# Performance work log

Measured on AMD Instinct MI355X. Metric: run time of the kernel, lower is better.

The kernel has to match this reference:

```python
import jax, jax.numpy as jnp
import numpy as np

GRAPH_SIZES = [864, 1728, 3456, 6912]
VERTEX_NUM = 6890
B, NZ, FC_DIM = 128, 128, 512
CH = [128, 128, 64, 32, 16]
EDGE_FACTOR = 6  # directed edges per node (triangle mesh)
LRELU = 0.2


def setup_inputs() -> dict:
    key = jax.random.key(0)
    ks = jax.random.split(key, 24)
    s = 0.02
    inp = {
        'x': jax.random.normal(ks[0], (B, NZ), jnp.float32),
        'fc_w1': s * jax.random.normal(ks[1], (NZ, FC_DIM), jnp.float32),
        'fc_b1': jnp.zeros((FC_DIM,), jnp.float32),
        'fc_w2': s * jax.random.normal(ks[2], (FC_DIM, GRAPH_SIZES[0] * CH[0]), jnp.float32),
        'fc_b2': jnp.zeros((GRAPH_SIZES[0] * CH[0],), jnp.float32),
    }
    # Chebyshev weights [K=3, C_in, C_out] per layer (+ final conv to 3)
    cio = [(CH[0], CH[1]), (CH[1], CH[2]), (CH[2], CH[3]), (CH[3], CH[4]), (CH[4], 3)]
    for i, (ci, co) in enumerate(cio):
        inp[f'W{i}'] = s * jax.random.normal(ks[3 + i], (3, ci, co), jnp.float32)
        inp[f'b{i}'] = jnp.zeros((co,), jnp.float32)
    # fixed edge lists per level
    for i, n in enumerate(GRAPH_SIZES):
        e = EDGE_FACTOR * n
        inp[f'edge{i}'] = jax.random.randint(ks[10 + i], (2, e), 0, n, dtype=jnp.int64)
    inp['perm_back'] = jax.random.randint(ks[20], (GRAPH_SIZES[-1],), 0, GRAPH_SIZES[-1], dtype=jnp.int64)
    return inp


def cheb_conv(x, edge_index, W, b, num_nodes):
    # PyG-style ChebConv with lambda_max=2: L_hat = L - I = -D^{-1/2} A D^{-1/2}
    src, dst = edge_index[0], edge_index[1]
    deg = jnp.zeros((num_nodes,), x.dtype).at[dst].add(jnp.ones(src.shape, x.dtype))
    dinv = jnp.where(deg > 0, 1.0 / jnp.sqrt(jnp.maximum(deg, 1.0)), 0.0)
    norm = -(dinv[src] * dinv[dst])  # [E]

    def prop(h):  # h: [B, N, C] -> L_hat @ h (gather + scatter-add over edges)
        msg = h[:, src, :] * norm[None, :, None]
        return jnp.zeros_like(h).at[:, dst, :].add(msg)

    Tx0 = x
    Tx1 = prop(Tx0)
    Tx2 = 2.0 * prop(Tx1) - Tx0
    out = (jnp.einsum('bnc,co->bno', Tx0, W[0])
           + jnp.einsum('bnc,co->bno', Tx1, W[1])
           + jnp.einsum('bnc,co->bno', Tx2, W[2]))
    return out + b


def lrelu(x):
    return jnp.where(x >= 0, x, LRELU * x)


def reference(x, fc_w1, fc_b1, fc_w2, fc_b2,
              W0, b0, W1, b1, W2, b2, W3, b3, W4, b4,
              edge0, edge1, edge2, edge3, perm_back):
    h = jax.nn.relu(x @ fc_w1 + fc_b1)
    h = h @ fc_w2 + fc_b2                      # dropout = identity (eval mode)
    h = h.reshape(h.shape[0], GRAPH_SIZES[0], -1)  # [B, 864, 128]
    edges = [edge0, edge1, edge2, edge3]
    Ws = [(W0, b0), (W1, b1), (W2, b2), (W3, b3)]
    for i in range(4):
        h = lrelu(cheb_conv(h, edges[i], Ws[i][0], Ws[i][1], GRAPH_SIZES[i]))
        if i < 3:
            h = jnp.repeat(h, 2, axis=1)       # Upsample(scale_factor=2) along nodes
    h = cheb_conv(h, edge3, W4, b4, GRAPH_SIZES[3])  # final conv to 3 coords
    h = h[:, perm_back, :]                      # perm_data gather
    return h[:, :VERTEX_NUM, :]
```

## Files before the change

kernel.cpp:

```cpp
#include <hip/hip_runtime.h>
#include <hip/hip_bf16.h>

#define DEVFN __device__ __forceinline__

__global__ void k_signal(float* out, float v) {
    if (threadIdx.x == 0 && blockIdx.x == 0) out[0] = v;
}

__global__ void k_detect64(const long long* __restrict__ p, int count, int* flag) {
    if (threadIdx.x == 0 && blockIdx.x == 0) {
        int ok = 1;
        for (int i = 0; i < count; i++) {
            long long v = p[i];
            if (v < 0 || v >= (1LL << 30)) { ok = 0; break; }
        }
        *flag = ok;
    }
}

__global__ __launch_bounds__(256) void k_cvt_idx(const void* __restrict__ p, int n,
                                                 const int* __restrict__ flag,
                                                 int* __restrict__ out) {
    int i = blockIdx.x * 256 + threadIdx.x;
    if (i >= n) return;
    if (*flag) out[i] = (int)((const long long*)p)[i];
    else       out[i] = ((const int*)p)[i];
}

__global__ __launch_bounds__(256) void k_fc1(const float* __restrict__ x,
                                             const float* __restrict__ w,
                                             const float* __restrict__ b,
                                             float* __restrict__ out) {
    int j = blockIdx.x * 256 + threadIdx.x;
    int m = blockIdx.y;
    float acc = b[j];
    const float* xr = x + m * 128;
    for (int k = 0; k < 128; k++)
        acc = fmaf(xr[k], w[k * 512 + j], acc);
    out[j * 128 + m] = fmaxf(acc, 0.f);
}

__global__ __launch_bounds__(256) void k_fc2_gemm4(const float* __restrict__ h1t,
                                                   const float* __restrict__ w,
                                                   const float* __restrict__ bias,
                                                   float* __restrict__ out) {
    const int N = 110592, K = 512;
    constexpr int KT = 32, NT = 128;
    __shared__ float At[KT * 128];
    __shared__ float Bt[KT * NT];

    const int tid = threadIdx.x;
    const int cg = tid & 15;
    const int rg = tid >> 4;
    const int nbase = blockIdx.x * NT;
    const int r0 = rg * 8;
    const int c0 = cg * 4;

    float acc[8][8];
#pragma unroll
    for (int j = 0; j < 4; j++) {
        float bj0 = bias[nbase + c0 + j];
        float bj1 = bias[nbase + 64 + c0 + j];
#pragma unroll
        for (int r = 0; r < 8; r++) { acc[r][j] = bj0; acc[r][j + 4] = bj1; }
    }

    for (int k0 = 0; k0 < K; k0 += KT) {
        __syncthreads();
#pragma unroll
        for (int it = 0; it < 4; it++) {
            int idx = tid + it * 256;
            int kk = idx >> 5, r4 = (idx & 31) * 4;
            *(float4*)(At + kk * 128 + r4) =
                *(const float4*)(h1t + (size_t)(k0 + kk) * 128 + r4);
        }
#pragma unroll
        for (int it = 0; it < 4; it++) {
            int idx = tid + it * 256;
            int kk = idx >> 5, c4 = (idx & 31) * 4;
            *(float4*)(Bt + kk * NT + c4) =
                *(const float4*)(w + (size_t)(k0 + kk) * N + nbase + c4);
        }
        __syncthreads();
#pragma unroll 8
        for (int k = 0; k < KT; k++) {
            float4 a0 = *(const float4*)(At + k * 128 + r0);
            float4 a1 = *(const float4*)(At + k * 128 + r0 + 4);
            float4 b0 = *(const float4*)(Bt + k * NT + c0);
            float4 b1 = *(const float4*)(Bt + k * NT + c0 + 64);
            float av[8] = {a0.x, a0.y, a0.z, a0.w, a1.x, a1.y, a1.z, a1.w};
            float bv[8] = {b0.x, b0.y, b0.z, b0.w, b1.x, b1.y, b1.z, b1.w};
#pragma unroll
            for (int r = 0; r < 8; r++)
#pragma unroll
                for (int j = 0; j < 8; j++)
                    acc[r][j] = fmaf(av[r], bv[j], acc[r][j]);
        }
    }

#pragma unroll
    for (int r = 0; r < 8; r++) {
        int m = r0 + r;
        float4 o0 = {acc[r][0], acc[r][1], acc[r][2], acc[r][3]};
        float4 o1 = {acc[r][4], acc[r][5], acc[r][6], acc[r][7]};
        *(float4*)(out + (size_t)m * N + nbase + c0) = o0;
        *(float4*)(out + (size_t)m * N + nbase + c0 + 64) = o1;
    }
}

__global__ __launch_bounds__(256) void k_zero_int(int* p, int n) {
    int i = blockIdx.x * 256 + threadIdx.x;
    if (i < n) p[i] = 0;
}

__global__ __launch_bounds__(256) void k_deg(const int* __restrict__ dst, int e,
                                             int* __restrict__ deg) {
    int i = blockIdx.x * 256 + threadIdx.x;
    if (i < e) atomicAdd(&deg[dst[i]], 1);
}

__global__ __launch_bounds__(256) void k_dinv(const int* __restrict__ deg,
                                              float* __restrict__ dinv, int n) {
    int i = blockIdx.x * 256 + threadIdx.x;
    if (i < n) dinv[i] = deg[i] > 0 ? 1.0f / sqrtf((float)deg[i]) : 0.0f;
}

__global__ __launch_bounds__(256) void k_scan(const int* __restrict__ deg,
                                              int* __restrict__ row_ptr, int n) {
    __shared__ int part[256];
    int tid = threadIdx.x;
    int per = (n + 255) / 256;
    int start = tid * per;
    int end = min(start + per, n);
    int s = 0;
    for (int i = start; i < end; i++) s += deg[i];
    part[tid] = s;
    __syncthreads();
    for (int off = 1; off < 256; off <<= 1) {
        int t = (tid >= off) ? part[tid - off] : 0;
        __syncthreads();
        part[tid] += t;
        __syncthreads();
    }
    int base = (tid == 0) ? 0 : part[tid - 1];
    int run = base;
    for (int i = start; i < end; i++) { row_ptr[i] = run; run += deg[i]; }
    if (tid == 255) row_ptr[n] = part[255];
}

__global__ __launch_bounds__(256) void k_fill(const int* __restrict__ src,
                                              const int* __restrict__ dst, int e,
                                              const int* __restrict__ row_ptr,
                                              int* __restrict__ cnt,
                                              const float* __restrict__ dinv,
                                              int* __restrict__ col, float* __restrict__ val) {
    int i = blockIdx.x * 256 + threadIdx.x;
    if (i >= e) return;
    int d = dst[i], s = src[i];
    int slot = row_ptr[d] + atomicAdd(&cnt[d], 1);
    col[slot] = s;
    val[slot] = -dinv[s] * dinv[d];
}

template <int CI, int MODE>
__global__ __launch_bounds__(256) void k_prop2(const float* __restrict__ h,
                                               const float* __restrict__ sub,
                                               const int* __restrict__ row_ptr,
                                               const int* __restrict__ col,
                                               const float* __restrict__ val,
                                               float* __restrict__ out, int n) {
    constexpr int C4 = CI / 4;
    constexpr int BY = 256 / C4;
    int c4 = threadIdx.x;
    int d = blockIdx.x;
    int b = blockIdx.y * BY + threadIdx.y;
    int p0 = row_ptr[d], p1 = row_ptr[d + 1];
    float4 acc = {0.f, 0.f, 0.f, 0.f};
    const float4* hb = (const float4*)h + (size_t)b * n * C4;
    for (int p = p0; p < p1; p++) {
        float vp = val[p];
        float4 hv = hb[(size_t)col[p] * C4 + c4];
        acc.x = fmaf(vp, hv.x, acc.x);
        acc.y = fmaf(vp, hv.y, acc.y);
        acc.z = fmaf(vp, hv.z, acc.z);
        acc.w = fmaf(vp, hv.w, acc.w);
    }
    size_t oi = ((size_t)b * n + d) * C4 + c4;
    if (MODE) {
        float4 s = ((const float4*)sub)[oi];
        acc.x = 2.f * acc.x - s.x;
        acc.y = 2.f * acc.y - s.y;
        acc.z = 2.f * acc.z - s.z;
        acc.w = 2.f * acc.w - s.w;
    }
    ((float4*)out)[oi] = acc;
}

template <int CI, int CO, bool REPEAT>
__global__ __launch_bounds__(256) void k_cheb_gemm3(const float* __restrict__ t0,
                                                    const float* __restrict__ t1,
                                                    const float* __restrict__ t2,
                                                    const float* __restrict__ W,
                                                    const float* __restrict__ bias,
                                                    float* __restrict__ out, int n) {
    constexpr int CGN = CO / 8;
    constexpr int MT = 1024 / CGN;
    constexpr int KT = 32, AST = 37;
    __shared__ float At[MT * AST];
    __shared__ float Wt_s[KT * CO];

    const int tid = threadIdx.x;
    const int cg = tid % CGN;
    const int rg = tid / CGN;
    const int m_base = blockIdx.x * MT;
    const int c0 = cg * 8;

    float acc[4][8];
#pragma unroll
    for (int jj = 0; jj < 8; jj++) {
        float bj = bias[c0 + jj];
#pragma unroll
        for (int r = 0; r < 4; r++) acc[r][jj] = bj;
    }

    const float* As[3] = {t0, t1, t2};
#pragma unroll 1
    for (int t = 0; t < 3; t++) {
        const float* A = As[t];
        const float* Wg = W + t * CI * CO;
#pragma unroll 1
        for (int k0 = 0; k0 < CI; k0 += KT) {
            __syncthreads();
#pragma unroll
            for (int it = 0; it < MT / 32; it++) {
                int idx = tid + it * 256;
                int row = idx >> 3, k4 = (idx & 7) * 4;
                float4 a = *(const float4*)(A + (size_t)(m_base + row) * CI + k0 + k4);
                float* dst = At + row * AST + k4;
                dst[0] = a.x; dst[1] = a.y; dst[2] = a.z; dst[3] = a.w;
            }
#pragma unroll
            for (int it = 0; it < (KT * CO) / 1024; it++) {
                int idx = tid + it * 256;
                int kk = idx / (CO / 4), c4 = (idx % (CO / 4)) * 4;
                *(float4*)(Wt_s + kk * CO + c4) =
                    *(const float4*)(Wg + (k0 + kk) * CO + c4);
            }
            __syncthreads();
#pragma unroll 4
            for (int k = 0; k < KT; k++) {
                float a0 = At[(rg * 4 + 0) * AST + k];
                float a1 = At[(rg * 4 + 1) * AST + k];
                float a2 = At[(rg * 4 + 2) * AST + k];
                float a3 = At[(rg * 4 + 3) * AST + k];
                float4 w0 = *(const float4*)(Wt_s + k * CO + c0);
                float4 w1 = *(const float4*)(Wt_s + k * CO + c0 + 4);
                float wv[8] = {w0.x, w0.y, w0.z, w0.w, w1.x, w1.y, w1.z, w1.w};
#pragma unroll
                for (int jj = 0; jj < 8; jj++) {
                    acc[0][jj] = fmaf(a0, wv[jj], acc[0][jj]);
                    acc[1][jj] = fmaf(a1, wv[jj], acc[1][jj]);
                    acc[2][jj] = fmaf(a2, wv[jj], acc[2][jj]);
                    acc[3][jj] = fmaf(a3, wv[jj], acc[3][jj]);
                }
            }
        }
    }

#pragma unroll
    for (int r = 0; r < 4; r++) {
        int m = m_base + rg * 4 + r;
#pragma unroll
        for (int jj = 0; jj < 8; jj++) {
            float v = acc[r][jj];
            acc[r][jj] = v >= 0.f ? v : 0.2f * v;
        }
        float4 o0 = {acc[r][0], acc[r][1], acc[r][2], acc[r][3]};
        float4 o1 = {acc[r][4], acc[r][5], acc[r][6], acc[r][7]};
        if (REPEAT) {
            int b = m / n, d = m - (m / n) * n;
            size_t ob = ((size_t)b * (2 * n) + 2 * d) * CO + c0;
            *(float4*)(out + ob) = o0;
            *(float4*)(out + ob + 4) = o1;
            *(float4*)(out + ob + CO) = o0;
            *(float4*)(out + ob + CO + 4) = o1;
        } else {
            *(float4*)(out + (size_t)m * CO + c0) = o0;
            *(float4*)(out + (size_t)m * CO + c0 + 4) = o1;
        }
    }
}

__global__ __launch_bounds__(256) void k_cheb_small(const float* __restrict__ t0,
                                                    const float* __restrict__ t1,
                                                    const float* __restrict__ t2,
                                                    const float* __restrict__ W,
                                                    const float* __restrict__ bias,
                                                    float* __restrict__ out) {
    constexpr int CI = 32, CO = 16, MT = 256, AST = 33;
    __shared__ float At[MT * AST];
    __shared__ float Ws[3 * CI * CO];

    const int tid = threadIdx.x;
    const int cg = tid & 1;
    const int rg = tid >> 1;
    const int c0 = cg * 8;
    const int m_base = blockIdx.x * MT;

    for (int i = tid; i < 384; i += 256)
        ((float4*)Ws)[i] = ((const float4*)W)[i];

    float acc[2][8];
#pragma unroll
    for (int jj = 0; jj < 8; jj++) {
        float bj = bias[c0 + jj];
        acc[0][jj] = bj; acc[1][jj] = bj;
    }

    const float* As[3] = {t0, t1, t2};
#pragma unroll 1
    for (int t = 0; t < 3; t++) {
        const float* A = As[t];
        __syncthreads();
#pragma unroll
        for (int it = 0; it < 8; it++) {
            int idx = tid + it * 256;
            int row = idx >> 3, k4 = (idx & 7) * 4;
            float4 a = *(const float4*)(A + (size_t)(m_base + row) * CI + k4);
            float* dst = At + row * AST + k4;
            dst[0] = a.x; dst[1] = a.y; dst[2] = a.z; dst[3] = a.w;
        }
        __syncthreads();
        const float* Wt = Ws + t * CI * CO;
#pragma unroll 8
        for (int k = 0; k < CI; k++) {
            float a0 = At[rg * AST + k];
            float a1 = At[(rg + 128) * AST + k];
            float4 w0 = *(const float4*)(Wt + k * CO + c0);
            float4 w1 = *(const float4*)(Wt + k * CO + c0 + 4);
            float wv[8] = {w0.x, w0.y, w0.z, w0.w, w1.x, w1.y, w1.z, w1.w};
#pragma unroll
            for (int jj = 0; jj < 8; jj++) {
                acc[0][jj] = fmaf(a0, wv[jj], acc[0][jj]);
                acc[1][jj] = fmaf(a1, wv[jj], acc[1][jj]);
            }
        }
    }

#pragma unroll
    for (int r = 0; r < 2; r++) {
        int m = m_base + rg + r * 128;
#pragma unroll
        for (int jj = 0; jj < 8; jj++) {
            float v = acc[r][jj];
            acc[r][jj] = v >= 0.f ? v : 0.2f * v;
        }
        float4 o0 = {acc[r][0], acc[r][1], acc[r][2], acc[r][3]};
        float4 o1 = {acc[r][4], acc[r][5], acc[r][6], acc[r][7]};
        *(float4*)(out + (size_t)m * CO + c0) = o0;
        *(float4*)(out + (size_t)m * CO + c0 + 4) = o1;
    }
}

__global__ __launch_bounds__(256) void k_final_conv(const float* __restrict__ t0,
                                                    const float* __restrict__ t1,
                                                    const float* __restrict__ t2,
                                                    const float* __restrict__ W,
                                                    const float* __restrict__ bias,
                                                    float* __restrict__ out, int M) {
    int m = blockIdx.x * 256 + threadIdx.x;
    if (m >= M) return;
    float a0 = bias[0], a1 = bias[1], a2 = bias[2];
    const float* hs[3] = {t0, t1, t2};
#pragma unroll
    for (int t = 0; t < 3; t++) {
        const float4* h4 = (const float4*)(hs[t] + (size_t)m * 16);
        const float* Wt = W + t * 48;
#pragma unroll
        for (int q = 0; q < 4; q++) {
            float4 hv = h4[q];
            const float* Wq = Wt + q * 12;
            a0 = fmaf(hv.x, Wq[0], a0); a1 = fmaf(hv.x, Wq[1], a1); a2 = fmaf(hv.x, Wq[2], a2);
            a0 = fmaf(hv.y, Wq[3], a0); a1 = fmaf(hv.y, Wq[4], a1); a2 = fmaf(hv.y, Wq[5], a2);
            a0 = fmaf(hv.z, Wq[6], a0); a1 = fmaf(hv.z, Wq[7], a1); a2 = fmaf(hv.z, Wq[8], a2);
            a0 = fmaf(hv.w, Wq[9], a0); a1 = fmaf(hv.w, Wq[10], a1); a2 = fmaf(hv.w, Wq[11], a2);
        }
    }
    out[(size_t)m * 3 + 0] = a0;
    out[(size_t)m * 3 + 1] = a1;
    out[(size_t)m * 3 + 2] = a2;
}

__global__ __launch_bounds__(256) void k_permute(const float* __restrict__ h,
                                                 const int* __restrict__ perm,
                                                 float* __restrict__ out) {
    const int V = 6890, N = 6912;
    int idx = blockIdx.x * 256 + threadIdx.x;
    if (idx >= 128 * V * 3) return;
    int c = idx % 3;
    int t = idx / 3;
    int v = t % V;
    int b = t / V;
    int p = perm[v];
    out[idx] = h[((size_t)b * N + p) * 3 + c];
}

extern "C" void kernel_launch(void* const* d_in, const int* in_sizes, int n_in,
                              void* d_out, int out_size, void* d_ws, size_t ws_size,
                              hipStream_t stream) {
    float* out = (float*)d_out;

    static const int SIZES[20] = {
        16384, 65536, 512, 56623104, 110592,
        49152, 128, 24576, 64, 6144, 32, 1536, 16, 144, 3,
        10368, 20736, 41472, 82944, 6912
    };
    const void* in[20];
    bool map_ok = (n_in == 20);
    if (map_ok) {
        for (int s = 0; s < 20; s++) {
            int found = -1;
            for (int i = 0; i < n_in; i++)
                if (in_sizes[i] == SIZES[s]) { found = i; break; }
            if (found < 0) { map_ok = false; break; }
            in[s] = d_in[found];
        }
    }
    if (!map_ok)
        for (int i = 0; i < 20 && i < n_in; i++) in[i] = d_in[i];

    const float* x     = (const float*)in[0];
    const float* fc_w1 = (const float*)in[1];
    const float* fc_b1 = (const float*)in[2];
    const float* fc_w2 = (const float*)in[3];
    const float* fc_b2 = (const float*)in[4];
    const float* W0 = (const float*)in[5];
    const float* b0 = (const float*)in[6];
    const float* W1 = (const float*)in[7];
    const float* b1 = (const float*)in[8];
    const float* W2 = (const float*)in[9];
    const float* b2 = (const float*)in[10];
    const float* W3 = (const float*)in[11];
    const float* b3 = (const float*)in[12];
    const float* W4 = (const float*)in[13];
    const float* b4 = (const float*)in[14];

    const size_t SZ = 28311552;
    float* ws = (float*)d_ws;
    float* buf0 = ws;
    float* buf1 = ws + SZ;
    float* buf2 = ws + 2 * SZ;
    float* buf3 = ws + 3 * SZ;
    float* h1   = ws + 4 * SZ;
    float* dinv = h1 + 65536;
    float* val  = dinv + 6912;
    int* ideg = (int*)(val + 41472);
    int* rowp = ideg + 6912;
    int* cnt  = rowp + 6913;
    int* col  = cnt + 6912;
    int* e0 = col + 41472;
    int* e1 = e0 + 10368;
    int* e2 = e1 + 20736;
    int* e3 = e2 + 41472;
    int* pm = e3 + 82944;
    int* flag = pm + 6912;
    size_t needed = (char*)(flag + 1) - (char*)d_ws;
    if (ws_size < needed) {
        k_signal<<<1, 64, 0, stream>>>(out, 1000.0f);
        return;
    }

    k_detect64<<<1, 64, 0, stream>>>((const long long*)in[15], 64, flag);
    k_cvt_idx<<<(10368 + 255) / 256, 256, 0, stream>>>(in[15], 10368, flag, e0);
    k_cvt_idx<<<(20736 + 255) / 256, 256, 0, stream>>>(in[16], 20736, flag, e1);
    k_cvt_idx<<<(41472 + 255) / 256, 256, 0, stream>>>(in[17], 41472, flag, e2);
    k_cvt_idx<<<(82944 + 255) / 256, 256, 0, stream>>>(in[18], 82944, flag, e3);
    k_cvt_idx<<<(6912 + 255) / 256, 256, 0, stream>>>(in[19], 6912, flag, pm);

    k_fc1<<<dim3(2, 128), 256, 0, stream>>>(x, fc_w1, fc_b1, h1);
    k_fc2_gemm4<<<864, 256, 0, stream>>>(h1, fc_w2, fc_b2, buf0);

    auto build = [&](const int* edge, int e, int n) {
        int nb_n = (n + 255) / 256, nb_e = (e + 255) / 256;
        k_zero_int<<<nb_n, 256, 0, stream>>>(ideg, n);
        k_zero_int<<<nb_n, 256, 0, stream>>>(cnt, n);
        k_deg<<<nb_e, 256, 0, stream>>>(edge + e, e, ideg);
        k_dinv<<<nb_n, 256, 0, stream>>>(ideg, dinv, n);
        k_scan<<<1, 256, 0, stream>>>(ideg, rowp, n);
        k_fill<<<nb_e, 256, 0, stream>>>(edge, edge + e, e, rowp, cnt, dinv, col, val);
    };

    build(e0, 6 * 864, 864);
    k_prop2<128, 0><<<dim3(864, 16), dim3(32, 8), 0, stream>>>(buf0, buf0, rowp, col, val, buf1, 864);
    k_prop2<128, 1><<<dim3(864, 16), dim3(32, 8), 0, stream>>>(buf1, buf0, rowp, col, val, buf2, 864);
    k_cheb_gemm3<128, 128, true><<<1728, 256, 0, stream>>>(buf0, buf1, buf2, W0, b0, buf3, 864);

    build(e1, 6 * 1728, 1728);
    k_prop2<128, 0><<<dim3(1728, 16), dim3(32, 8), 0, stream>>>(buf3, buf3, rowp, col, val, buf1, 1728);
    k_prop2<128, 1><<<dim3(1728, 16), dim3(32, 8), 0, stream>>>(buf1, buf3, rowp, col, val, buf2, 1728);
    k_cheb_gemm3<128, 64, true><<<1728, 256, 0, stream>>>(buf3, buf1, buf2, W1, b1, buf0, 1728);

    build(e2, 6 * 3456, 3456);
    k_prop2<64, 0><<<dim3(3456, 8), dim3(16, 16), 0, stream>>>(buf0, buf0, rowp, col, val, buf1, 3456);
    k_prop2<64, 1><<<dim3(3456, 8), dim3(16, 16), 0, stream>>>(buf1, buf0, rowp, col, val, buf2, 3456);
    k_cheb_gemm3<64, 32, true><<<1728, 256, 0, stream>>>(buf0, buf1, buf2, W2, b2, buf3, 3456);

    build(e3, 6 * 6912, 6912);
    k_prop2<32, 0><<<dim3(6912, 4), dim3(8, 32), 0, stream>>>(buf3, buf3, rowp, col, val, buf1, 6912);
    k_prop2<32, 1><<<dim3(6912, 4), dim3(8, 32), 0, stream>>>(buf1, buf3, rowp, col, val, buf2, 6912);
    k_cheb_small<<<3456, 256, 0, stream>>>(buf3, buf1, buf2, W3, b3, buf0);

    k_prop2<16, 0><<<dim3(6912, 2), dim3(4, 64), 0, stream>>>(buf0, buf0, rowp, col, val, buf1, 6912);
    k_prop2<16, 1><<<dim3(6912, 2), dim3(4, 64), 0, stream>>>(buf1, buf0, rowp, col, val, buf2, 6912);
    k_final_conv<<<(884736 + 255) / 256, 256, 0, stream>>>(buf0, buf1, buf2, W4, b4, buf3, 884736);

    int tot = 128 * 6890 * 3;
    k_permute<<<(tot + 255) / 256, 256, 0, stream>>>(buf3, pm, out);

    if (!map_ok) k_signal<<<1, 64, 0, stream>>>(out, 2000.0f);
}
```

Before: 2.068 ms.

## Double-buffer fc2 GEMM tiles with direct global-to-LDS async loads

Rewrites the large fc2 GEMM to use two LDS buffers with a smaller K tile. The next tile is staged while the current one is computed, and it is staged with the amdgcn global_load_lds builtin, which writes global data straight into shared memory without a register round-trip. The aim is to hide global load latency and cut the barrier-bound stalls between load and compute phases. In exchange it relies on the compiler placing the correct vmcnt waits before barriers for the async LDS writes. The smaller K tile also doubles the number of barriers.

```diff
diff --git a/kernel.cpp b/kernel.cpp
--- a/kernel.cpp
+++ b/kernel.cpp
@@ -2,6 +2,26 @@
 #include <hip/hip_bf16.h>
 
 #define DEVFN __device__ __forceinline__
+
+#if defined(__has_builtin)
+#if __has_builtin(__builtin_amdgcn_global_load_lds)
+#define HAS_GLL 1
+#else
+#define HAS_GLL 0
+#endif
+#else
+#define HAS_GLL 0
+#endif
+
+DEVFN void gload_lds16(const float* g, float* l) {
+#if HAS_GLL
+    __builtin_amdgcn_global_load_lds(
+        (const __attribute__((address_space(1))) void*)g,
+        (__attribute__((address_space(3))) void*)l, 16, 0, 0);
+#else
+    *(float4*)l = *(const float4*)g;
+#endif
+}
 
 __global__ void k_signal(float* out, float v) {
     if (threadIdx.x == 0 && blockIdx.x == 0) out[0] = v;
@@ -40,14 +60,14 @@
     out[j * 128 + m] = fmaxf(acc, 0.f);
 }
 
-__global__ __launch_bounds__(256) void k_fc2_gemm4(const float* __restrict__ h1t,
+__global__ __launch_bounds__(256) void k_fc2_gemm6(const float* __restrict__ h1t,
                                                    const float* __restrict__ w,
                                                    const float* __restrict__ bias,
                                                    float* __restrict__ out) {
-    const int N = 110592, K = 512;
-    constexpr int KT = 32, NT = 128;
-    __shared__ float At[KT * 128];
-    __shared__ float Bt[KT * NT];
+    const int N = 110592;
+    constexpr int KT = 16, NT = 128;
+    __shared__ float At[2 * KT * 128];
+    __shared__ float Bt[2 * KT * NT];
 
     const int tid = threadIdx.x;
     const int cg = tid & 15;
@@ -65,29 +85,31 @@
         for (int r = 0; r < 8; r++) { acc[r][j] = bj0; acc[r][j + 4] = bj1; }
     }
 
-    for (int k0 = 0; k0 < K; k0 += KT) {
-        __syncthreads();
-#pragma unroll
-        for (int it = 0; it < 4; it++) {
+    auto stage = [&](int buf, int k0) {
+#pragma unroll
+        for (int it = 0; it < 2; it++) {
             int idx = tid + it * 256;
-            int kk = idx >> 5, r4 = (idx & 31) * 4;
-            *(float4*)(At + kk * 128 + r4) =
-                *(const float4*)(h1t + (size_t)(k0 + kk) * 128 + r4);
-        }
-#pragma unroll
-        for (int it = 0; it < 4; it++) {
+            gload_lds16(h1t + (size_t)k0 * 128 + idx * 4,
+                        At + buf * (KT * 128) + idx * 4);
+        }
+#pragma unroll
+        for (int it = 0; it < 2; it++) {
             int idx = tid + it * 256;
             int kk = idx >> 5, c4 = (idx & 31) * 4;
-            *(float4*)(Bt + kk * NT + c4) =
-                *(const float4*)(w + (size_t)(k0 + kk) * N + nbase + c4);
-        }
-        __syncthreads();
-#pragma unroll 8
+            gload_lds16(w + (size_t)(k0 + kk) * N + nbase + c4,
+                        Bt + buf * (KT * NT) + idx * 4);
+        }
+    };
+
+    auto compute = [&](int buf) {
+        const float* Ab = At + buf * (KT * 128);
+        const float* Bb = Bt + buf * (KT * NT);
+#pragma unroll
         for (int k = 0; k < KT; k++) {
-            float4 a0 = *(const float4*)(At + k * 128 + r0);
-            float4 a1 = *(const float4*)(At + k * 128 + r0 + 4);
-            float4 b0 = *(const float4*)(Bt + k * NT + c0);
-            float4 b1 = *(const float4*)(Bt + k * NT + c0 + 64);
+            float4 a0 = *(const float4*)(Ab + k * 128 + r0);
+            float4 a1 = *(const float4*)(Ab + k * 128 + r0 + 4);
+            float4 b0 = *(const float4*)(Bb + k * NT + c0);
+            float4 b1 = *(const float4*)(Bb + k * NT + c0 + 64);
             float av[8] = {a0.x, a0.y, a0.z, a0.w, a1.x, a1.y, a1.z, a1.w};
             float bv[8] = {b0.x, b0.y, b0.z, b0.w, b1.x, b1.y, b1.z, b1.w};
 #pragma unroll
@@ -96,7 +118,23 @@
                 for (int j = 0; j < 8; j++)
                     acc[r][j] = fmaf(av[r], bv[j], acc[r][j]);
         }
-    }
+    };
+
+    stage(0, 0);
+    __syncthreads();
+#pragma unroll 1
+    for (int t = 0; t + 2 < 32; t += 2) {
+        stage(1, (t + 1) * KT);
+        compute(0);
+        __syncthreads();
+        stage(0, (t + 2) * KT);
+        compute(1);
+        __syncthreads();
+    }
+    stage(1, 31 * KT);
+    compute(0);
+    __syncthreads();
+    compute(1);
 
 #pragma unroll
     for (int r = 0; r < 8; r++) {
@@ -478,7 +516,7 @@
     k_cvt_idx<<<(6912 + 255) / 256, 256, 0, stream>>>(in[19], 6912, flag, pm);
 
     k_fc1<<<dim3(2, 128), 256, 0, stream>>>(x, fc_w1, fc_b1, h1);
-    k_fc2_gemm4<<<864, 256, 0, stream>>>(h1, fc_w2, fc_b2, buf0);
+    k_fc2_gemm6<<<864, 256, 0, stream>>>(h1, fc_w2, fc_b2, buf0);
 
     auto build = [&](const int* edge, int e, int n) {
         int nb_n = (n + 255) / 256, nb_e = (e + 255) / 256;
```

After: 2.176 ms. +5.2%, slower.
